# Kernel tuning notes

Measured on AMD Instinct MI355X. Metric: run time of the kernel, lower is better.

## Reference

```python
import jax, jax.numpy as jnp
import numpy as np

H0, W0 = 256, 256
B = 8
N_EV = 100000
N_PARAMS = 4000000
SMOOTHNESS_WEIGHT = 0.5
WEIGHT_DECAY_WEIGHT = 1e-4


def setup_inputs() -> dict:
    key = jax.random.key(0)
    ks = jax.random.split(key, 11)
    d = {}
    for i in range(4):
        s = 2 ** (3 - i)
        d['flow%d' % i] = jax.random.normal(ks[i], (B, 2, H0 // s, W0 // s), jnp.float32)
    d['xs'] = jax.random.randint(ks[4], (B, N_EV), 0, W0).astype(jnp.int32)
    d['ys'] = jax.random.randint(ks[5], (B, N_EV), 0, H0).astype(jnp.int32)
    # timestamps sorted ascending so t[-1]/t[0] are the last/first event times
    d['ts'] = jnp.sort(jax.random.uniform(ks[6], (B, N_EV), jnp.float32), axis=1)
    # polarity in {-1, +1}
    d['ps'] = (2 * jax.random.randint(ks[7], (B, N_EV), 0, 2) - 1).astype(jnp.int32)
    d['frame'] = jax.random.normal(ks[8], (B, 1, H0, W0), jnp.float32)
    d['frame_'] = jax.random.normal(ks[9], (B, 1, H0, W0), jnp.float32)
    d['params'] = jax.random.normal(ks[10], (N_PARAMS,), jnp.float32) * 0.01
    return d


def _event_loss(x, y, t, mask, flow, forward):
    # x, y: int32 [N] in-range coords for this flow scale; t: float [N];
    # mask: bool [N] selecting the polarity subset; flow: [2, H, W].
    # Masked events contribute zero weight instead of being sliced out
    # (shape-stable equivalent of torch boolean indexing).
    eps = jnp.finfo(flow.dtype).eps
    H, W = flow.shape[1], flow.shape[2]
    n = t.shape[0]
    mf = mask.astype(flow.dtype)
    if forward:
        t_ref = t[n - 1 - jnp.argmax(mask[::-1])]  # t[-1] of masked subset
        t_ = t_ref - t + eps
    else:
        t_ref = t[jnp.argmax(mask)]  # t[0] of masked subset
        t_ = t_ref - t - eps
    fx = flow[0, y, x]
    fy = flow[1, y, x]
    x_ = jnp.clip(x.astype(flow.dtype) + t_ * fx, 0.0, W - 1.0)
    y_ = jnp.clip(y.astype(flow.dtype) + t_ * fy, 0.0, H - 1.0)
    x0 = jnp.floor(x_); x1 = x0 + 1.0
    y0 = jnp.floor(y_); y1 = y0 + 1.0
    x0w = x_ - x0; x1w = x1 - x_
    y0w = y_ - y0; y1w = y1 - y_
    tm = t * mf
    Ta = x0w * y0w * tm
    Tb = x1w * y0w * tm
    Tc = x0w * y1w * tm
    Td = x1w * y1w * tm
    x1i = jnp.minimum(x1, W - 1.0).astype(jnp.int32)
    y1i = jnp.minimum(y1, H - 1.0).astype(jnp.int32)
    x0i = x0.astype(jnp.int32); y0i = y0.astype(jnp.int32)
    Ia = x1i + y1i * W
    Ib = x0i + y1i * W
    Ic = x1i + y0i * W
    Id = x0i + y0i * W
    idxs = jnp.concatenate([Ia, Ib, Ic, Id])
    vals = jnp.concatenate([Ta, Tb, Tc, Td])
    den = jnp.zeros(H * W, flow.dtype).at[idxs].add(jnp.tile(mf, 4))
    num = jnp.zeros(H * W, flow.dtype).at[idxs].add(vals)
    r = num / (den + eps)
    return jnp.sum(jnp.sqrt(r * r + 1e-06))


def _compute_event_flow_loss(xs, ys, ts, ps, flows):
    total = jnp.float32(0.0)
    pos = ps == 1
    neg = ps == -1
    for fi, flow in enumerate(flows):  # 4 scales, structurally distinct shapes
        scale = 2 ** (3 - fi)
        x = (xs.astype(jnp.float32) / scale).astype(jnp.int32)
        y = (ys.astype(jnp.float32) / scale).astype(jnp.int32)
        for mask in (pos, neg):
            for fwd in (True, False):
                f = lambda xb, yb, tb, mb, fb, fwd=fwd: _event_loss(xb, yb, tb, mb, fb, fwd)
                total = total + jnp.sum(jax.vmap(f)(x, y, ts, mask, flow))
    return total


def _charbonnier(d):
    # alpha=0.45, epsilon=1e-3 -> epsilon**2 = 1e-6
    return jnp.mean((d * d + 1e-06) ** 0.45)


def _smoothness(flow):
    lr = _charbonnier(flow[..., :, 1:] - flow[..., :, :-1])
    ud = _charbonnier(flow[..., 1:, :] - flow[..., :-1, :])
    d1 = _charbonnier(flow[..., 1:, 1:] - flow[..., :-1, :-1])
    d2 = _charbonnier(flow[..., :-1, 1:] - flow[..., 1:, :-1])
    return (lr + ud + d1 + d2) / 4.0


def reference(flow0, flow1, flow2, flow3, xs, ys, ts, ps, frame, frame_, params):
    flows = [flow0, flow1, flow2, flow3]
    weight_decay_loss = jnp.sum(params ** 2) / 2.0 * WEIGHT_DECAY_WEIGHT
    smoothness_loss = sum(_smoothness(f) for f in flows) * (SMOOTHNESS_WEIGHT / 4.0)
    event_loss = _compute_event_flow_loss(xs, ys, ts, ps, flows)
    return weight_decay_loss + event_loss + smoothness_loss * 200.0
```

## Files before the change

### kernel.cpp

```cpp
#include <hip/hip_runtime.h>
#include <math.h>
#include <limits.h>

#define NEV 100000
#define NB 8
#define NSL 32
#define SLEV (NEV / NSL)
#define F32EPS 1.1920929e-7f
#define SCALE 524288.0f
#define INV_SCALE (1.0f/524288.0f)

typedef unsigned long long u64;

#define BINS_BYTES 6400000
#define OFF_BINSTART 6400000
#define OFF_TREF     6401056
#define OFF_FI0P     6401184
#define OFF_FI1P     8498336
#define OFF_HISTG    12692640
#define OFF_CURSG    12823712
#define OFF_MMG      12954784

__device__ __forceinline__ void lds_add64(u64* p, u64 v) {
    __hip_atomic_fetch_add(p, v, __ATOMIC_RELAXED, __HIP_MEMORY_SCOPE_WORKGROUP);
}
__device__ __forceinline__ int lds_add32(int* p, int v) {
    return __hip_atomic_fetch_add(p, v, __ATOMIC_RELAXED, __HIP_MEMORY_SCOPE_WORKGROUP);
}

__global__ __launch_bounds__(256) void k_hist(
    const int* __restrict__ ys, const int* __restrict__ ps,
    int* __restrict__ histG, int* __restrict__ mmG) {
    int bid = blockIdx.x;
    int b = bid & 7;
    int sl = bid >> 3;
    int tid = threadIdx.x;
    int w = tid >> 6, lane = tid & 63;

    const int* yb = ys + b * NEV + sl * SLEV;
    const int* pb = ps + b * NEV + sl * SLEV;

    __shared__ int hist[4][32];
    __shared__ int mm[4];
    if (tid < 128) hist[tid >> 5][tid & 31] = 0;
    if (tid == 0) { mm[0] = INT_MAX; mm[1] = -1; mm[2] = INT_MAX; mm[3] = -1; }
    __syncthreads();

    int mnP = INT_MAX, mxP = -1, mnN = INT_MAX, mxN = -1;
    int gbase = sl * SLEV;
    for (int i = w * 64 + lane; i < SLEV; i += 256) {
        int p = pb[i];
        int y = yb[i];
        int m = (p == 1) ? 0 : 1;
        lds_add32(&hist[w][m * 16 + (y >> 4)], 1);
        int gi = gbase + i;
        if (m == 0) { mnP = min(mnP, gi); mxP = max(mxP, gi); }
        else        { mnN = min(mnN, gi); mxN = max(mxN, gi); }
    }
    for (int o = 32; o > 0; o >>= 1) {
        mnP = min(mnP, __shfl_down(mnP, o, 64));
        mxP = max(mxP, __shfl_down(mxP, o, 64));
        mnN = min(mnN, __shfl_down(mnN, o, 64));
        mxN = max(mxN, __shfl_down(mxN, o, 64));
    }
    if (lane == 0) {
        atomicMin(&mm[0], mnP); atomicMax(&mm[1], mxP);
        atomicMin(&mm[2], mnN); atomicMax(&mm[3], mxN);
    }
    __syncthreads();
    if (tid < 128) histG[(bid * 4 + (tid >> 5)) * 32 + (tid & 31)] = hist[tid >> 5][tid & 31];
    if (tid < 4)   mmG[bid * 4 + tid] = mm[tid];
}

__global__ __launch_bounds__(256) void k_scan(
    const int* __restrict__ histG, const int* __restrict__ mmG,
    const float* __restrict__ ts,
    int* __restrict__ cursG, int* __restrict__ binStart,
    float* __restrict__ tref, float* __restrict__ out) {
    int tid = threadIdx.x;
    int b = tid >> 5, bin = tid & 31;
    __shared__ int tot[8][32];
    __shared__ int bs[8][33];

    int s = 0;
    for (int sl = 0; sl < NSL; ++sl) {
        int bid = sl * 8 + b;
        #pragma unroll
        for (int w = 0; w < 4; ++w) s += histG[(bid * 4 + w) * 32 + bin];
    }
    tot[b][bin] = s;
    __syncthreads();

    if (tid < 8) {
        int run = 0;
        for (int k = 0; k < 32; ++k) { bs[tid][k] = run; run += tot[tid][k]; }
        bs[tid][32] = run;
    }
    __syncthreads();
    if (bin == 0 && b == 0) out[0] = 0.0f;
    binStart[b * 33 + bin] = bs[b][bin];
    if (tid < 8) binStart[tid * 33 + 32] = bs[tid][32];

    int run = bs[b][bin];
    for (int sl = 0; sl < NSL; ++sl) {
        int bid = sl * 8 + b;
        #pragma unroll
        for (int w = 0; w < 4; ++w) {
            int idx = (bid * 4 + w) * 32 + bin;
            int h = histG[idx];
            cursG[idx] = run;
            run += h;
        }
    }

    if (tid < 8) {
        int mnP = INT_MAX, mxP = -1, mnN = INT_MAX, mxN = -1;
        for (int sl = 0; sl < NSL; ++sl) {
            const int* m = mmG + (sl * 8 + tid) * 4;
            mnP = min(mnP, m[0]); mxP = max(mxP, m[1]);
            mnN = min(mnN, m[2]); mxN = max(mxN, m[3]);
        }
        const float* tb = ts + tid * NEV;
        int fP = (mnP == INT_MAX) ? 0 : mnP;
        int lP = (mxP < 0) ? (NEV - 1) : mxP;
        int fN = (mnN == INT_MAX) ? 0 : mnN;
        int lN = (mxN < 0) ? (NEV - 1) : mxN;
        tref[tid * 4 + 0] = tb[lP];
        tref[tid * 4 + 1] = tb[fP];
        tref[tid * 4 + 2] = tb[lN];
        tref[tid * 4 + 3] = tb[fN];
    }
}

__global__ __launch_bounds__(256) void k_scatter(
    const int* __restrict__ xs, const int* __restrict__ ys,
    const float* __restrict__ ts, const int* __restrict__ ps,
    const int* __restrict__ cursG, uint2* __restrict__ bins) {
    int bid = blockIdx.x;
    int b = bid & 7;
    int sl = bid >> 3;
    int tid = threadIdx.x;
    int w = tid >> 6, lane = tid & 63;

    const int*   xb = xs + b * NEV + sl * SLEV;
    const int*   yb = ys + b * NEV + sl * SLEV;
    const float* tb = ts + b * NEV + sl * SLEV;
    const int*   pb = ps + b * NEV + sl * SLEV;
    uint2* ob = bins + b * NEV;

    __shared__ int curs[4][32];
    if (tid < 128) curs[tid >> 5][tid & 31] = cursG[(bid * 4 + (tid >> 5)) * 32 + (tid & 31)];
    __syncthreads();

    for (int i = w * 64 + lane; i < SLEV; i += 256) {
        int p = pb[i];
        int x = xb[i];
        int y = yb[i];
        float t = tb[i];
        int m = (p == 1) ? 0 : 1;
        int bin = m * 16 + (y >> 4);
        int pos = lds_add32(&curs[w][bin], 1);
        ob[pos] = make_uint2((unsigned)(x | (y << 8)), __float_as_uint(t));
    }
}

__global__ __launch_bounds__(1024) void k_splat(
    const float* __restrict__ f0, const float* __restrict__ f1,
    const float* __restrict__ f2, const float* __restrict__ f3,
    const uint2* __restrict__ bins, const int* __restrict__ binStart,
    const float* __restrict__ tref,
    u64* __restrict__ fi0P, u64* __restrict__ fi1P,
    float* __restrict__ out) {
    __shared__ u64 acc[8192];
    __shared__ float red[16];

    int tid = threadIdx.x;
    int bid = blockIdx.x;
    int b = bid & 7;
    int rm = bid >> 3;
    int m = rm & 1;
    int role = rm >> 1;
    int bm = b * 2 + m;

    int fi, row0 = 0, nrows, lo, hi, slice = 0, nslice = 1, mode;
    if (role < 8)       { fi = 0; mode = 0; slice = role;      nslice = 8; nrows = 32; lo = 0; hi = 15; }
    else if (role < 12) { fi = 1; mode = 0; slice = role - 8;  nslice = 4; nrows = 64; lo = 0; hi = 15; }
    else if (role < 20) { int c = role - 12; fi = 2; mode = 1; row0 = 16 * c; nrows = 16;
                          lo = max(0, 2 * c - 1); hi = min(15, 2 * c + 2); }
    else                { int c = role - 20; fi = 3; mode = 1; row0 = 16 * c; nrows = 16;
                          lo = max(0, c - 1); hi = min(15, c + 1); }

    int W = 32 << fi;
    int sh = 3 - fi;
    int planeN = (fi == 0) ? 1024 : (fi == 1) ? 4096 : nrows * W;
    int used = (fi == 0) ? 8192 : 2 * planeN;
    int rowEnd = row0 + nrows;
    float Wm1 = (float)(W - 1);

    const float* flow = (fi == 0) ? f0 : (fi == 1) ? f1 : (fi == 2) ? f2 : f3;
    const float* fxp = flow + (size_t)b * 2 * W * W;
    const float* fyp = fxp + W * W;

    for (int i = tid; i < used; i += 1024) acc[i] = 0ULL;
    __syncthreads();

    float trF = tref[b * 4 + m * 2 + 0];
    float trB = tref[b * 4 + m * 2 + 1];

    int s0 = binStart[b * 33 + m * 16 + lo];
    int e0 = binStart[b * 33 + m * 16 + hi + 1];
    const uint2* eb = bins + b * NEV;

    int rep = (fi == 0) ? (((tid >> 4) & 3) * 2048) : 0;

    for (int i = s0 + slice * 1024 + tid; i < e0; i += nslice * 1024) {
        uint2 ev = eb[i];
        int x = ev.x & 255;
        int y = (ev.x >> 8) & 255;
        float t = __uint_as_float(ev.y);
        int xi = x >> sh, yi = y >> sh;
        float fx = fxp[yi * W + xi];
        float fy = fyp[yi * W + xi];
        float tF = trF - t + F32EPS;
        float tB = trB - t - F32EPS;
        #pragma unroll
        for (int dir = 0; dir < 2; ++dir) {
            float t_ = dir ? tB : tF;
            float x_ = fminf(fmaxf((float)xi + t_ * fx, 0.0f), Wm1);
            float y_ = fminf(fmaxf((float)yi + t_ * fy, 0.0f), Wm1);
            float x0f = floorf(x_), y0f = floorf(y_);
            float x0w = x_ - x0f, x1w = 1.0f - x0w;
            float y0w = y_ - y0f, y1w = 1.0f - y0w;
            int x0i = (int)x0f, y0i = (int)y0f;
            int x1i = min(x0i + 1, W - 1);
            int y1i = min(y0i + 1, W - 1);
            u64 Pa = (1ULL << 32) | (u64)(unsigned)(x0w * y0w * t * SCALE);
            u64 Pb = (1ULL << 32) | (u64)(unsigned)(x1w * y0w * t * SCALE);
            u64 Pc = (1ULL << 32) | (u64)(unsigned)(x0w * y1w * t * SCALE);
            u64 Pd = (1ULL << 32) | (u64)(unsigned)(x1w * y1w * t * SCALE);
            int base = rep + dir * planeN;
            if (mode == 0) {
                int r1 = base + y1i * W;
                int r0 = base + y0i * W;
                lds_add64(&acc[r1 + x1i], Pa);
                lds_add64(&acc[r1 + x0i], Pb);
                lds_add64(&acc[r0 + x1i], Pc);
                lds_add64(&acc[r0 + x0i], Pd);
            } else {
                if (y1i >= row0 && y1i < rowEnd) {
                    int r = base + (y1i - row0) * W;
                    lds_add64(&acc[r + x1i], Pa);
                    lds_add64(&acc[r + x0i], Pb);
                }
                if (y0i >= row0 && y0i < rowEnd) {
                    int r = base + (y0i - row0) * W;
                    lds_add64(&acc[r + x1i], Pc);
                    lds_add64(&acc[r + x0i], Pd);
                }
            }
        }
    }
    __syncthreads();

    if (mode == 0) {
        if (fi == 0) {
            for (int j = tid; j < 2048; j += 1024)
                fi0P[(bm * 8 + slice) * 2048 + j] =
                    acc[j] + acc[j + 2048] + acc[j + 4096] + acc[j + 6144];
        } else {
            for (int j = tid; j < 8192; j += 1024)
                fi1P[(bm * 4 + slice) * 8192 + j] = acc[j];
        }
        return;
    }

    float s = 0.0f;
    for (int j = tid; j < used; j += 1024) {
        u64 v = acc[j];
        float num = (float)(unsigned)(v & 0xffffffffULL) * INV_SCALE;
        float den = (float)(unsigned)(v >> 32);
        float r = num / (den + F32EPS);
        s += sqrtf(r * r + 1e-6f);
    }
    for (int o = 32; o > 0; o >>= 1) s += __shfl_down(s, o, 64);
    if ((tid & 63) == 0) red[tid >> 6] = s;
    __syncthreads();
    if (tid == 0) {
        float tot = 0.0f;
        for (int w2 = 0; w2 < 16; ++w2) tot += red[w2];
        atomicAdd(out, tot);
    }
}

__global__ __launch_bounds__(256) void k_merge(const u64* __restrict__ fi0P,
                                               const u64* __restrict__ fi1P,
                                               float* __restrict__ out) {
    int idx = blockIdx.x * 256 + threadIdx.x;
    u64 v = 0;
    if (idx < 32768) {
        int bm = idx >> 11, j = idx & 2047;
        const u64* p = fi0P + (bm * 8) * 2048 + j;
        #pragma unroll
        for (int s = 0; s < 8; ++s) v += p[s * 2048];
    } else {
        int r = idx - 32768;
        int bm = r >> 13, j = r & 8191;
        const u64* p = fi1P + (bm * 4) * 8192 + j;
        #pragma unroll
        for (int s = 0; s < 4; ++s) v += p[s * 8192];
    }
    float num = (float)(unsigned)(v & 0xffffffffULL) * INV_SCALE;
    float den = (float)(unsigned)(v >> 32);
    float r = num / (den + F32EPS);
    float s = sqrtf(r * r + 1e-6f);
    for (int o = 32; o > 0; o >>= 1) s += __shfl_down(s, o, 64);
    __shared__ float red[4];
    if ((threadIdx.x & 63) == 0) red[threadIdx.x >> 6] = s;
    __syncthreads();
    if (threadIdx.x == 0)
        atomicAdd(out, red[0] + red[1] + red[2] + red[3]);
}

__global__ __launch_bounds__(256) void k_misc(
    const float* __restrict__ params, int nP,
    const float* __restrict__ f0, const float* __restrict__ f1,
    const float* __restrict__ f2, const float* __restrict__ f3,
    float* __restrict__ out) {
    float s = 0.0f;
    int gstride = gridDim.x * blockDim.x;
    int gtid = blockIdx.x * blockDim.x + threadIdx.x;

    int n4 = nP >> 2;
    const float4* p4 = (const float4*)params;
    float w = 0.0f;
    for (int i = gtid; i < n4; i += gstride) {
        float4 v = p4[i];
        w += v.x * v.x + v.y * v.y + v.z * v.z + v.w * v.w;
    }
    if (gtid == 0) for (int i = n4 * 4; i < nP; ++i) w += params[i] * params[i];
    s += w * 5e-5f;

    const int nTot = 1392640;
    for (int idx = gtid; idx < nTot; idx += gstride) {
        int fi, off, logW;
        if (idx < 16384)       { fi = 0; off = 0;      logW = 5; }
        else if (idx < 81920)  { fi = 1; off = 16384;  logW = 6; }
        else if (idx < 344064) { fi = 2; off = 81920;  logW = 7; }
        else                   { fi = 3; off = 344064; logW = 8; }
        const float* f = (fi == 0) ? f0 : (fi == 1) ? f1 : (fi == 2) ? f2 : f3;
        int W = 1 << logW;
        int local = idx - off;
        int x = local & (W - 1);
        int y = (local >> logW) & (W - 1);
        float c_lr = 6.25f / (float)(16 * W * (W - 1));
        float c_dd = 6.25f / (float)(16 * (W - 1) * (W - 1));
        float v = f[local];
        bool xok = x < W - 1;
        bool yok = y < W - 1;
        float vr = xok ? f[local + 1] : 0.0f;
        float vd = yok ? f[local + W] : 0.0f;
        if (xok) { float d = vr - v; s += c_lr * __powf(d * d + 1e-6f, 0.45f); }
        if (yok) { float d = vd - v; s += c_lr * __powf(d * d + 1e-6f, 0.45f); }
        if (xok && yok) {
            float d1 = f[local + W + 1] - v;
            s += c_dd * __powf(d1 * d1 + 1e-6f, 0.45f);
            float d2 = vr - vd;
            s += c_dd * __powf(d2 * d2 + 1e-6f, 0.45f);
        }
    }

    for (int o = 32; o > 0; o >>= 1) s += __shfl_down(s, o, 64);
    __shared__ float red[4];
    if ((threadIdx.x & 63) == 0) red[threadIdx.x >> 6] = s;
    __syncthreads();
    if (threadIdx.x == 0)
        atomicAdd(out, red[0] + red[1] + red[2] + red[3]);
}

extern "C" void kernel_launch(void* const* d_in, const int* in_sizes, int n_in,
                              void* d_out, int out_size, void* d_ws, size_t ws_size,
                              hipStream_t stream) {
    const float* f0 = (const float*)d_in[0];
    const float* f1 = (const float*)d_in[1];
    const float* f2 = (const float*)d_in[2];
    const float* f3 = (const float*)d_in[3];
    const int*   xs = (const int*)d_in[4];
    const int*   ys = (const int*)d_in[5];
    const float* ts = (const float*)d_in[6];
    const int*   ps = (const int*)d_in[7];
    const float* params = (const float*)d_in[10];
    float* out = (float*)d_out;

    char* ws = (char*)d_ws;
    uint2* bins     = (uint2*)ws;
    int*   binStart = (int*)(ws + OFF_BINSTART);
    float* tref     = (float*)(ws + OFF_TREF);
    u64*   fi0P     = (u64*)(ws + OFF_FI0P);
    u64*   fi1P     = (u64*)(ws + OFF_FI1P);
    int*   histG    = (int*)(ws + OFF_HISTG);
    int*   cursG    = (int*)(ws + OFF_CURSG);
    int*   mmG      = (int*)(ws + OFF_MMG);

    hipLaunchKernelGGL(k_hist, dim3(NB * NSL), dim3(256), 0, stream, ys, ps, histG, mmG);
    hipLaunchKernelGGL(k_scan, dim3(1), dim3(256), 0, stream,
                       histG, mmG, ts, cursG, binStart, tref, out);
    hipLaunchKernelGGL(k_scatter, dim3(NB * NSL), dim3(256), 0, stream,
                       xs, ys, ts, ps, cursG, bins);
    hipLaunchKernelGGL(k_splat, dim3(576), dim3(1024), 0, stream,
                       f0, f1, f2, f3, bins, binStart, tref, fi0P, fi1P, out);
    hipLaunchKernelGGL(k_merge, dim3(640), dim3(256), 0, stream, fi0P, fi1P, out);
    hipLaunchKernelGGL(k_misc, dim3(1024), dim3(256), 0, stream,
                       params, in_sizes[10], f0, f1, f2, f3, out);
}
```

Before: 182.6 us.

## Fuse all six passes into one cooperative kernel with grid syncs

Replaces the six separate launches (hist, scan, scatter, splat, merge, misc) with a single cooperative kernel of 256 blocks of 1024 threads, separated by grid-wide syncs. The scan runs on 8 blocks while the other blocks compute weight decay and smoothness concurrently, and the splat work is repartitioned into two units per block with fewer slices for the coarsest scale. This removes kernel launch gaps and the serial single-block scan stall. In exchange it adds grid-sync costs, and every phase is limited to 256 co-resident blocks.

```diff
diff --git a/kernel.cpp b/kernel.cpp
--- a/kernel.cpp
+++ b/kernel.cpp
@@ -1,9 +1,11 @@
 #include <hip/hip_runtime.h>
+#include <hip/hip_cooperative_groups.h>
 #include <math.h>
 #include <limits.h>
 
+namespace cg = cooperative_groups;
+
 #define NEV 100000
-#define NB 8
 #define NSL 32
 #define SLEV (NEV / NSL)
 #define F32EPS 1.1920929e-7f
@@ -12,14 +14,13 @@
 
 typedef unsigned long long u64;
 
-#define BINS_BYTES 6400000
 #define OFF_BINSTART 6400000
 #define OFF_TREF     6401056
 #define OFF_FI0P     6401184
-#define OFF_FI1P     8498336
-#define OFF_HISTG    12692640
-#define OFF_CURSG    12823712
-#define OFF_MMG      12954784
+#define OFF_FI1P     7449760
+#define OFF_HISTG    11644064
+#define OFF_CURSG    12168352
+#define OFF_MMB      12692640
 
 __device__ __forceinline__ void lds_add64(u64* p, u64 v) {
     __hip_atomic_fetch_add(p, v, __ATOMIC_RELAXED, __HIP_MEMORY_SCOPE_WORKGROUP);
@@ -28,353 +29,345 @@
     return __hip_atomic_fetch_add(p, v, __ATOMIC_RELAXED, __HIP_MEMORY_SCOPE_WORKGROUP);
 }
 
-__global__ __launch_bounds__(256) void k_hist(
-    const int* __restrict__ ys, const int* __restrict__ ps,
-    int* __restrict__ histG, int* __restrict__ mmG) {
-    int bid = blockIdx.x;
-    int b = bid & 7;
-    int sl = bid >> 3;
-    int tid = threadIdx.x;
-    int w = tid >> 6, lane = tid & 63;
-
-    const int* yb = ys + b * NEV + sl * SLEV;
-    const int* pb = ps + b * NEV + sl * SLEV;
-
-    __shared__ int hist[4][32];
-    __shared__ int mm[4];
-    if (tid < 128) hist[tid >> 5][tid & 31] = 0;
-    if (tid == 0) { mm[0] = INT_MAX; mm[1] = -1; mm[2] = INT_MAX; mm[3] = -1; }
-    __syncthreads();
-
-    int mnP = INT_MAX, mxP = -1, mnN = INT_MAX, mxN = -1;
-    int gbase = sl * SLEV;
-    for (int i = w * 64 + lane; i < SLEV; i += 256) {
-        int p = pb[i];
-        int y = yb[i];
-        int m = (p == 1) ? 0 : 1;
-        lds_add32(&hist[w][m * 16 + (y >> 4)], 1);
-        int gi = gbase + i;
-        if (m == 0) { mnP = min(mnP, gi); mxP = max(mxP, gi); }
-        else        { mnN = min(mnN, gi); mxN = max(mxN, gi); }
-    }
-    for (int o = 32; o > 0; o >>= 1) {
-        mnP = min(mnP, __shfl_down(mnP, o, 64));
-        mxP = max(mxP, __shfl_down(mxP, o, 64));
-        mnN = min(mnN, __shfl_down(mnN, o, 64));
-        mxN = max(mxN, __shfl_down(mxN, o, 64));
-    }
-    if (lane == 0) {
-        atomicMin(&mm[0], mnP); atomicMax(&mm[1], mxP);
-        atomicMin(&mm[2], mnN); atomicMax(&mm[3], mxN);
-    }
-    __syncthreads();
-    if (tid < 128) histG[(bid * 4 + (tid >> 5)) * 32 + (tid & 31)] = hist[tid >> 5][tid & 31];
-    if (tid < 4)   mmG[bid * 4 + tid] = mm[tid];
-}
-
-__global__ __launch_bounds__(256) void k_scan(
-    const int* __restrict__ histG, const int* __restrict__ mmG,
-    const float* __restrict__ ts,
-    int* __restrict__ cursG, int* __restrict__ binStart,
-    float* __restrict__ tref, float* __restrict__ out) {
-    int tid = threadIdx.x;
-    int b = tid >> 5, bin = tid & 31;
-    __shared__ int tot[8][32];
-    __shared__ int bs[8][33];
-
-    int s = 0;
-    for (int sl = 0; sl < NSL; ++sl) {
-        int bid = sl * 8 + b;
-        #pragma unroll
-        for (int w = 0; w < 4; ++w) s += histG[(bid * 4 + w) * 32 + bin];
-    }
-    tot[b][bin] = s;
-    __syncthreads();
-
-    if (tid < 8) {
-        int run = 0;
-        for (int k = 0; k < 32; ++k) { bs[tid][k] = run; run += tot[tid][k]; }
-        bs[tid][32] = run;
-    }
-    __syncthreads();
-    if (bin == 0 && b == 0) out[0] = 0.0f;
-    binStart[b * 33 + bin] = bs[b][bin];
-    if (tid < 8) binStart[tid * 33 + 32] = bs[tid][32];
-
-    int run = bs[b][bin];
-    for (int sl = 0; sl < NSL; ++sl) {
-        int bid = sl * 8 + b;
-        #pragma unroll
-        for (int w = 0; w < 4; ++w) {
-            int idx = (bid * 4 + w) * 32 + bin;
-            int h = histG[idx];
-            cursG[idx] = run;
-            run += h;
-        }
-    }
-
-    if (tid < 8) {
-        int mnP = INT_MAX, mxP = -1, mnN = INT_MAX, mxN = -1;
-        for (int sl = 0; sl < NSL; ++sl) {
-            const int* m = mmG + (sl * 8 + tid) * 4;
-            mnP = min(mnP, m[0]); mxP = max(mxP, m[1]);
-            mnN = min(mnN, m[2]); mxN = max(mxN, m[3]);
-        }
-        const float* tb = ts + tid * NEV;
-        int fP = (mnP == INT_MAX) ? 0 : mnP;
-        int lP = (mxP < 0) ? (NEV - 1) : mxP;
-        int fN = (mnN == INT_MAX) ? 0 : mnN;
-        int lN = (mxN < 0) ? (NEV - 1) : mxN;
-        tref[tid * 4 + 0] = tb[lP];
-        tref[tid * 4 + 1] = tb[fP];
-        tref[tid * 4 + 2] = tb[lN];
-        tref[tid * 4 + 3] = tb[fN];
-    }
-}
-
-__global__ __launch_bounds__(256) void k_scatter(
+__global__ __launch_bounds__(1024, 4) void k_fused(
+    const float* __restrict__ f0, const float* __restrict__ f1,
+    const float* __restrict__ f2, const float* __restrict__ f3,
     const int* __restrict__ xs, const int* __restrict__ ys,
     const float* __restrict__ ts, const int* __restrict__ ps,
-    const int* __restrict__ cursG, uint2* __restrict__ bins) {
-    int bid = blockIdx.x;
-    int b = bid & 7;
-    int sl = bid >> 3;
-    int tid = threadIdx.x;
-    int w = tid >> 6, lane = tid & 63;
-
-    const int*   xb = xs + b * NEV + sl * SLEV;
-    const int*   yb = ys + b * NEV + sl * SLEV;
-    const float* tb = ts + b * NEV + sl * SLEV;
-    const int*   pb = ps + b * NEV + sl * SLEV;
-    uint2* ob = bins + b * NEV;
-
-    __shared__ int curs[4][32];
-    if (tid < 128) curs[tid >> 5][tid & 31] = cursG[(bid * 4 + (tid >> 5)) * 32 + (tid & 31)];
-    __syncthreads();
-
-    for (int i = w * 64 + lane; i < SLEV; i += 256) {
-        int p = pb[i];
-        int x = xb[i];
-        int y = yb[i];
-        float t = tb[i];
-        int m = (p == 1) ? 0 : 1;
-        int bin = m * 16 + (y >> 4);
-        int pos = lds_add32(&curs[w][bin], 1);
-        ob[pos] = make_uint2((unsigned)(x | (y << 8)), __float_as_uint(t));
+    const float* __restrict__ params, int nP,
+    uint2* __restrict__ bins, int* __restrict__ binStart,
+    float* __restrict__ tref, u64* __restrict__ fi0P, u64* __restrict__ fi1P,
+    int* __restrict__ histG, int* __restrict__ cursG, int* __restrict__ mmB,
+    float* __restrict__ out)
+{
+    cg::grid_group grid = cg::this_grid();
+    __shared__ u64 acc[8192];
+    int*   shi = (int*)acc;
+    float* shf = (float*)acc;
+
+    const int tid  = threadIdx.x;
+    const int bid  = blockIdx.x;
+    const int w    = tid >> 6;
+    const int lane = tid & 63;
+
+    {
+        const int b = bid & 7, sl = bid >> 3;
+        const int* yb = ys + b * NEV + sl * SLEV;
+        const int* pb = ps + b * NEV + sl * SLEV;
+        if (tid < 512) shi[tid] = 0;
+        if (tid >= 512 && tid < 516) shi[tid] = (tid & 1) ? -1 : INT_MAX;
+        if (bid == 0 && tid == 1023) out[0] = 0.0f;
+        __syncthreads();
+
+        int mnP = INT_MAX, mxP = -1, mnN = INT_MAX, mxN = -1;
+        const int gbase = sl * SLEV;
+        for (int i = tid; i < SLEV; i += 1024) {
+            int p = pb[i], y = yb[i];
+            int m = (p == 1) ? 0 : 1;
+            lds_add32(&shi[w * 32 + m * 16 + (y >> 4)], 1);
+            int gi = gbase + i;
+            if (m == 0) { mnP = min(mnP, gi); mxP = max(mxP, gi); }
+            else        { mnN = min(mnN, gi); mxN = max(mxN, gi); }
+        }
+        for (int o = 32; o > 0; o >>= 1) {
+            mnP = min(mnP, __shfl_down(mnP, o, 64));
+            mxP = max(mxP, __shfl_down(mxP, o, 64));
+            mnN = min(mnN, __shfl_down(mnN, o, 64));
+            mxN = max(mxN, __shfl_down(mxN, o, 64));
+        }
+        if (lane == 0) {
+            atomicMin(&shi[512], mnP); atomicMax(&shi[513], mxP);
+            atomicMin(&shi[514], mnN); atomicMax(&shi[515], mxN);
+        }
+        __syncthreads();
+        if (tid < 512) histG[bid * 512 + tid] = shi[tid];
+        if (tid < 4)   mmB[bid * 4 + tid] = shi[512 + tid];
     }
-}
-
-__global__ __launch_bounds__(1024) void k_splat(
-    const float* __restrict__ f0, const float* __restrict__ f1,
-    const float* __restrict__ f2, const float* __restrict__ f3,
-    const uint2* __restrict__ bins, const int* __restrict__ binStart,
-    const float* __restrict__ tref,
-    u64* __restrict__ fi0P, u64* __restrict__ fi1P,
-    float* __restrict__ out) {
-    __shared__ u64 acc[8192];
-    __shared__ float red[16];
-
-    int tid = threadIdx.x;
-    int bid = blockIdx.x;
-    int b = bid & 7;
-    int rm = bid >> 3;
-    int m = rm & 1;
-    int role = rm >> 1;
-    int bm = b * 2 + m;
-
-    int fi, row0 = 0, nrows, lo, hi, slice = 0, nslice = 1, mode;
-    if (role < 8)       { fi = 0; mode = 0; slice = role;      nslice = 8; nrows = 32; lo = 0; hi = 15; }
-    else if (role < 12) { fi = 1; mode = 0; slice = role - 8;  nslice = 4; nrows = 64; lo = 0; hi = 15; }
-    else if (role < 20) { int c = role - 12; fi = 2; mode = 1; row0 = 16 * c; nrows = 16;
-                          lo = max(0, 2 * c - 1); hi = min(15, 2 * c + 2); }
-    else                { int c = role - 20; fi = 3; mode = 1; row0 = 16 * c; nrows = 16;
-                          lo = max(0, c - 1); hi = min(15, c + 1); }
-
-    int W = 32 << fi;
-    int sh = 3 - fi;
-    int planeN = (fi == 0) ? 1024 : (fi == 1) ? 4096 : nrows * W;
-    int used = (fi == 0) ? 8192 : 2 * planeN;
-    int rowEnd = row0 + nrows;
-    float Wm1 = (float)(W - 1);
-
-    const float* flow = (fi == 0) ? f0 : (fi == 1) ? f1 : (fi == 2) ? f2 : f3;
-    const float* fxp = flow + (size_t)b * 2 * W * W;
-    const float* fyp = fxp + W * W;
-
-    for (int i = tid; i < used; i += 1024) acc[i] = 0ULL;
-    __syncthreads();
-
-    float trF = tref[b * 4 + m * 2 + 0];
-    float trB = tref[b * 4 + m * 2 + 1];
-
-    int s0 = binStart[b * 33 + m * 16 + lo];
-    int e0 = binStart[b * 33 + m * 16 + hi + 1];
-    const uint2* eb = bins + b * NEV;
-
-    int rep = (fi == 0) ? (((tid >> 4) & 3) * 2048) : 0;
-
-    for (int i = s0 + slice * 1024 + tid; i < e0; i += nslice * 1024) {
-        uint2 ev = eb[i];
-        int x = ev.x & 255;
-        int y = (ev.x >> 8) & 255;
-        float t = __uint_as_float(ev.y);
-        int xi = x >> sh, yi = y >> sh;
-        float fx = fxp[yi * W + xi];
-        float fy = fyp[yi * W + xi];
-        float tF = trF - t + F32EPS;
-        float tB = trB - t - F32EPS;
+    grid.sync();
+
+    if (bid < 8) {
+        const int b = bid;
+        const int sl = tid >> 5, bin = tid & 31;
+        int s = 0;
         #pragma unroll
-        for (int dir = 0; dir < 2; ++dir) {
-            float t_ = dir ? tB : tF;
-            float x_ = fminf(fmaxf((float)xi + t_ * fx, 0.0f), Wm1);
-            float y_ = fminf(fmaxf((float)yi + t_ * fy, 0.0f), Wm1);
-            float x0f = floorf(x_), y0f = floorf(y_);
-            float x0w = x_ - x0f, x1w = 1.0f - x0w;
-            float y0w = y_ - y0f, y1w = 1.0f - y0w;
-            int x0i = (int)x0f, y0i = (int)y0f;
-            int x1i = min(x0i + 1, W - 1);
-            int y1i = min(y0i + 1, W - 1);
-            u64 Pa = (1ULL << 32) | (u64)(unsigned)(x0w * y0w * t * SCALE);
-            u64 Pb = (1ULL << 32) | (u64)(unsigned)(x1w * y0w * t * SCALE);
-            u64 Pc = (1ULL << 32) | (u64)(unsigned)(x0w * y1w * t * SCALE);
-            u64 Pd = (1ULL << 32) | (u64)(unsigned)(x1w * y1w * t * SCALE);
-            int base = rep + dir * planeN;
-            if (mode == 0) {
-                int r1 = base + y1i * W;
-                int r0 = base + y0i * W;
-                lds_add64(&acc[r1 + x1i], Pa);
-                lds_add64(&acc[r1 + x0i], Pb);
-                lds_add64(&acc[r0 + x1i], Pc);
-                lds_add64(&acc[r0 + x0i], Pd);
+        for (int wv = 0; wv < 16; ++wv)
+            s += histG[((sl * 8 + b) * 16 + wv) * 32 + bin];
+        shi[sl * 32 + bin] = s;
+        __syncthreads();
+        if (tid < 32) {
+            int run = 0;
+            for (int g = 0; g < 32; ++g) {
+                int v = shi[g * 32 + tid];
+                shi[1024 + g * 32 + tid] = run; run += v;
+            }
+            shi[2048 + tid] = run;
+        }
+        __syncthreads();
+        if (tid == 0) {
+            int run = 0;
+            for (int k = 0; k < 32; ++k) {
+                shi[2080 + k] = run; binStart[b * 33 + k] = run;
+                run += shi[2048 + k];
+            }
+            binStart[b * 33 + 32] = run;
+        }
+        __syncthreads();
+        {
+            int run = shi[2080 + bin] + shi[1024 + sl * 32 + bin];
+            #pragma unroll
+            for (int wv = 0; wv < 16; ++wv) {
+                int idx = ((sl * 8 + b) * 16 + wv) * 32 + bin;
+                int h = histG[idx];
+                cursG[idx] = run; run += h;
+            }
+        }
+        if (tid < 4) {
+            int c = tid;
+            int v = (c == 0 || c == 2) ? INT_MAX : -1;
+            for (int sl2 = 0; sl2 < 32; ++sl2) {
+                int x = mmB[(sl2 * 8 + b) * 4 + c];
+                v = (c == 0 || c == 2) ? min(v, x) : max(v, x);
+            }
+            shi[2112 + c] = v;
+        }
+        __syncthreads();
+        if (tid == 0) {
+            const float* tb = ts + b * NEV;
+            int mnP = shi[2112], mxP = shi[2113], mnN = shi[2114], mxN = shi[2115];
+            int fP = (mnP == INT_MAX) ? 0 : mnP;
+            int lP = (mxP < 0) ? (NEV - 1) : mxP;
+            int fN = (mnN == INT_MAX) ? 0 : mnN;
+            int lN = (mxN < 0) ? (NEV - 1) : mxN;
+            tref[b * 4 + 0] = tb[lP];
+            tref[b * 4 + 1] = tb[fP];
+            tref[b * 4 + 2] = tb[lN];
+            tref[b * 4 + 3] = tb[fN];
+        }
+    } else {
+        float s = 0.0f;
+        const int gtid = (bid - 8) * 1024 + tid;
+        const int gstride = 248 * 1024;
+
+        int n4 = nP >> 2;
+        const float4* p4 = (const float4*)params;
+        float wsum = 0.0f;
+        for (int i = gtid; i < n4; i += gstride) {
+            float4 v = p4[i];
+            wsum += v.x * v.x + v.y * v.y + v.z * v.z + v.w * v.w;
+        }
+        if (gtid == 0) for (int i = n4 * 4; i < nP; ++i) wsum += params[i] * params[i];
+        s += wsum * 5e-5f;
+
+        const int nTot = 1392640;
+        for (int idx = gtid; idx < nTot; idx += gstride) {
+            int fi, off, logW;
+            if (idx < 16384)       { fi = 0; off = 0;      logW = 5; }
+            else if (idx < 81920)  { fi = 1; off = 16384;  logW = 6; }
+            else if (idx < 344064) { fi = 2; off = 81920;  logW = 7; }
+            else                   { fi = 3; off = 344064; logW = 8; }
+            const float* f = (fi == 0) ? f0 : (fi == 1) ? f1 : (fi == 2) ? f2 : f3;
+            int W = 1 << logW;
+            int local = idx - off;
+            int x = local & (W - 1);
+            int y = (local >> logW) & (W - 1);
+            float c_lr = 6.25f / (float)(16 * W * (W - 1));
+            float c_dd = 6.25f / (float)(16 * (W - 1) * (W - 1));
+            float v = f[local];
+            bool xok = x < W - 1;
+            bool yok = y < W - 1;
+            float vr = xok ? f[local + 1] : 0.0f;
+            float vd = yok ? f[local + W] : 0.0f;
+            if (xok) { float d = vr - v; s += c_lr * __powf(d * d + 1e-6f, 0.45f); }
+            if (yok) { float d = vd - v; s += c_lr * __powf(d * d + 1e-6f, 0.45f); }
+            if (xok && yok) {
+                float d1 = f[local + W + 1] - v;
+                s += c_dd * __powf(d1 * d1 + 1e-6f, 0.45f);
+                float d2 = vr - vd;
+                s += c_dd * __powf(d2 * d2 + 1e-6f, 0.45f);
+            }
+        }
+        for (int o = 32; o > 0; o >>= 1) s += __shfl_down(s, o, 64);
+        __syncthreads();
+        if (lane == 0) shf[w] = s;
+        __syncthreads();
+        if (tid == 0) {
+            float tot = 0.0f;
+            for (int k = 0; k < 16; ++k) tot += shf[k];
+            atomicAdd(out, tot);
+        }
+    }
+    grid.sync();
+
+    {
+        const int b = bid & 7, sl = bid >> 3;
+        const int*   xb  = xs + b * NEV + sl * SLEV;
+        const int*   yb  = ys + b * NEV + sl * SLEV;
+        const float* tb2 = ts + b * NEV + sl * SLEV;
+        const int*   pb  = ps + b * NEV + sl * SLEV;
+        uint2* ob = bins + b * NEV;
+
+        if (tid < 512) shi[tid] = cursG[bid * 512 + tid];
+        __syncthreads();
+        for (int i = tid; i < SLEV; i += 1024) {
+            int p = pb[i], x = xb[i], y = yb[i];
+            float t = tb2[i];
+            int m = (p == 1) ? 0 : 1;
+            int bin = m * 16 + (y >> 4);
+            int pos = lds_add32(&shi[w * 32 + bin], 1);
+            ob[pos] = make_uint2((unsigned)(x | (y << 8)), __float_as_uint(t));
+        }
+    }
+    grid.sync();
+
+    for (int u = 0; u < 2; ++u) {
+        const int unit = bid + u * 256;
+        const int b = unit & 7;
+        const int rm = unit >> 3;
+        const int m = rm & 1;
+        const int role = rm >> 1;
+        const int bm = b * 2 + m;
+
+        int fi, row0 = 0, nrows, lo, hi, slice = 0, nslice = 1, mode;
+        if (role < 4)       { fi = 0; mode = 0; slice = role;     nslice = 4; nrows = 32; lo = 0; hi = 15; }
+        else if (role < 8)  { fi = 1; mode = 0; slice = role - 4; nslice = 4; nrows = 64; lo = 0; hi = 15; }
+        else if (role < 16) { int c = role - 8;  fi = 2; mode = 1; row0 = 16 * c; nrows = 16;
+                              lo = max(0, 2 * c - 1); hi = min(15, 2 * c + 2); }
+        else                { int c = role - 16; fi = 3; mode = 1; row0 = 16 * c; nrows = 16;
+                              lo = max(0, c - 1); hi = min(15, c + 1); }
+
+        const int W = 32 << fi;
+        const int sh = 3 - fi;
+        const int planeN = (fi == 0) ? 1024 : (fi == 1) ? 4096 : nrows * W;
+        const int used = (fi == 0) ? 8192 : 2 * planeN;
+        const int rowEnd = row0 + nrows;
+        const float Wm1 = (float)(W - 1);
+
+        const float* flow = (fi == 0) ? f0 : (fi == 1) ? f1 : (fi == 2) ? f2 : f3;
+        const float* fxp = flow + (size_t)b * 2 * W * W;
+        const float* fyp = fxp + W * W;
+
+        __syncthreads();
+        for (int i = tid; i < used; i += 1024) acc[i] = 0ULL;
+        __syncthreads();
+
+        const float trF = tref[b * 4 + m * 2 + 0];
+        const float trB = tref[b * 4 + m * 2 + 1];
+        const int s0 = binStart[b * 33 + m * 16 + lo];
+        const int e0 = binStart[b * 33 + m * 16 + hi + 1];
+        const uint2* eb = bins + b * NEV;
+        const int rep = (fi == 0) ? (((tid >> 4) & 3) * 2048) : 0;
+
+        for (int i = s0 + slice * 1024 + tid; i < e0; i += nslice * 1024) {
+            uint2 ev = eb[i];
+            int x = ev.x & 255;
+            int y = (ev.x >> 8) & 255;
+            float t = __uint_as_float(ev.y);
+            int xi = x >> sh, yi = y >> sh;
+            float fx = fxp[yi * W + xi];
+            float fy = fyp[yi * W + xi];
+            float tF = trF - t + F32EPS;
+            float tB = trB - t - F32EPS;
+            #pragma unroll
+            for (int dir = 0; dir < 2; ++dir) {
+                float t_ = dir ? tB : tF;
+                float x_ = fminf(fmaxf((float)xi + t_ * fx, 0.0f), Wm1);
+                float y_ = fminf(fmaxf((float)yi + t_ * fy, 0.0f), Wm1);
+                float x0f = floorf(x_), y0f = floorf(y_);
+                float x0w = x_ - x0f, x1w = 1.0f - x0w;
+                float y0w = y_ - y0f, y1w = 1.0f - y0w;
+                int x0i = (int)x0f, y0i = (int)y0f;
+                int x1i = min(x0i + 1, W - 1);
+                int y1i = min(y0i + 1, W - 1);
+                u64 Pa = (1ULL << 32) | (u64)(unsigned)(x0w * y0w * t * SCALE);
+                u64 Pb = (1ULL << 32) | (u64)(unsigned)(x1w * y0w * t * SCALE);
+                u64 Pc = (1ULL << 32) | (u64)(unsigned)(x0w * y1w * t * SCALE);
+                u64 Pd = (1ULL << 32) | (u64)(unsigned)(x1w * y1w * t * SCALE);
+                int base = rep + dir * planeN;
+                if (mode == 0) {
+                    int r1 = base + y1i * W;
+                    int r0 = base + y0i * W;
+                    lds_add64(&acc[r1 + x1i], Pa);
+                    lds_add64(&acc[r1 + x0i], Pb);
+                    lds_add64(&acc[r0 + x1i], Pc);
+                    lds_add64(&acc[r0 + x0i], Pd);
+                } else {
+                    if (y1i >= row0 && y1i < rowEnd) {
+                        int r = base + (y1i - row0) * W;
+                        lds_add64(&acc[r + x1i], Pa);
+                        lds_add64(&acc[r + x0i], Pb);
+                    }
+                    if (y0i >= row0 && y0i < rowEnd) {
+                        int r = base + (y0i - row0) * W;
+                        lds_add64(&acc[r + x1i], Pc);
+                        lds_add64(&acc[r + x0i], Pd);
+                    }
+                }
+            }
+        }
+        __syncthreads();
+
+        if (mode == 0) {
+            if (fi == 0) {
+                for (int j = tid; j < 2048; j += 1024)
+                    fi0P[(bm * 4 + slice) * 2048 + j] =
+                        acc[j] + acc[j + 2048] + acc[j + 4096] + acc[j + 6144];
             } else {
-                if (y1i >= row0 && y1i < rowEnd) {
-                    int r = base + (y1i - row0) * W;
-                    lds_add64(&acc[r + x1i], Pa);
-                    lds_add64(&acc[r + x0i], Pb);
-                }
-                if (y0i >= row0 && y0i < rowEnd) {
-                    int r = base + (y0i - row0) * W;
-                    lds_add64(&acc[r + x1i], Pc);
-                    lds_add64(&acc[r + x0i], Pd);
-                }
+                for (int j = tid; j < 8192; j += 1024)
+                    fi1P[(bm * 4 + slice) * 8192 + j] = acc[j];
+            }
+        } else {
+            float s = 0.0f;
+            for (int j = tid; j < used; j += 1024) {
+                u64 v = acc[j];
+                float num = (float)(unsigned)(v & 0xffffffffULL) * INV_SCALE;
+                float den = (float)(unsigned)(v >> 32);
+                float r = num / (den + F32EPS);
+                s += sqrtf(r * r + 1e-6f);
+            }
+            for (int o = 32; o > 0; o >>= 1) s += __shfl_down(s, o, 64);
+            __syncthreads();
+            if (lane == 0) shf[w] = s;
+            __syncthreads();
+            if (tid == 0) {
+                float tot = 0.0f;
+                for (int k = 0; k < 16; ++k) tot += shf[k];
+                atomicAdd(out, tot);
             }
         }
     }
-    __syncthreads();
-
-    if (mode == 0) {
-        if (fi == 0) {
-            for (int j = tid; j < 2048; j += 1024)
-                fi0P[(bm * 8 + slice) * 2048 + j] =
-                    acc[j] + acc[j + 2048] + acc[j + 4096] + acc[j + 6144];
-        } else {
-            for (int j = tid; j < 8192; j += 1024)
-                fi1P[(bm * 4 + slice) * 8192 + j] = acc[j];
-        }
-        return;
+    grid.sync();
+
+    {
+        const int idx = bid * 1024 + tid;
+        if (idx < 163840) {
+            u64 v = 0;
+            if (idx < 32768) {
+                int bm = idx >> 11, j = idx & 2047;
+                const u64* p = fi0P + (bm * 4) * 2048 + j;
+                #pragma unroll
+                for (int s2 = 0; s2 < 4; ++s2) v += p[s2 * 2048];
+            } else {
+                int r = idx - 32768;
+                int bm = r >> 13, j = r & 8191;
+                const u64* p = fi1P + (bm * 4) * 8192 + j;
+                #pragma unroll
+                for (int s2 = 0; s2 < 4; ++s2) v += p[s2 * 8192];
+            }
+            float num = (float)(unsigned)(v & 0xffffffffULL) * INV_SCALE;
+            float den = (float)(unsigned)(v >> 32);
+            float r2 = num / (den + F32EPS);
+            float sv = sqrtf(r2 * r2 + 1e-6f);
+            for (int o = 32; o > 0; o >>= 1) sv += __shfl_down(sv, o, 64);
+            __syncthreads();
+            if (lane == 0) shf[w] = sv;
+            __syncthreads();
+            if (tid == 0) {
+                float tot = 0.0f;
+                for (int k = 0; k < 16; ++k) tot += shf[k];
+                atomicAdd(out, tot);
+            }
+        }
     }
-
-    float s = 0.0f;
-    for (int j = tid; j < used; j += 1024) {
-        u64 v = acc[j];
-        float num = (float)(unsigned)(v & 0xffffffffULL) * INV_SCALE;
-        float den = (float)(unsigned)(v >> 32);
-        float r = num / (den + F32EPS);
-        s += sqrtf(r * r + 1e-6f);
-    }
-    for (int o = 32; o > 0; o >>= 1) s += __shfl_down(s, o, 64);
-    if ((tid & 63) == 0) red[tid >> 6] = s;
-    __syncthreads();
-    if (tid == 0) {
-        float tot = 0.0f;
-        for (int w2 = 0; w2 < 16; ++w2) tot += red[w2];
-        atomicAdd(out, tot);
-    }
-}
-
-__global__ __launch_bounds__(256) void k_merge(const u64* __restrict__ fi0P,
-                                               const u64* __restrict__ fi1P,
-                                               float* __restrict__ out) {
-    int idx = blockIdx.x * 256 + threadIdx.x;
-    u64 v = 0;
-    if (idx < 32768) {
-        int bm = idx >> 11, j = idx & 2047;
-        const u64* p = fi0P + (bm * 8) * 2048 + j;
-        #pragma unroll
-        for (int s = 0; s < 8; ++s) v += p[s * 2048];
-    } else {
-        int r = idx - 32768;
-        int bm = r >> 13, j = r & 8191;
-        const u64* p = fi1P + (bm * 4) * 8192 + j;
-        #pragma unroll
-        for (int s = 0; s < 4; ++s) v += p[s * 8192];
-    }
-    float num = (float)(unsigned)(v & 0xffffffffULL) * INV_SCALE;
-    float den = (float)(unsigned)(v >> 32);
-    float r = num / (den + F32EPS);
-    float s = sqrtf(r * r + 1e-6f);
-    for (int o = 32; o > 0; o >>= 1) s += __shfl_down(s, o, 64);
-    __shared__ float red[4];
-    if ((threadIdx.x & 63) == 0) red[threadIdx.x >> 6] = s;
-    __syncthreads();
-    if (threadIdx.x == 0)
-        atomicAdd(out, red[0] + red[1] + red[2] + red[3]);
-}
-
-__global__ __launch_bounds__(256) void k_misc(
-    const float* __restrict__ params, int nP,
-    const float* __restrict__ f0, const float* __restrict__ f1,
-    const float* __restrict__ f2, const float* __restrict__ f3,
-    float* __restrict__ out) {
-    float s = 0.0f;
-    int gstride = gridDim.x * blockDim.x;
-    int gtid = blockIdx.x * blockDim.x + threadIdx.x;
-
-    int n4 = nP >> 2;
-    const float4* p4 = (const float4*)params;
-    float w = 0.0f;
-    for (int i = gtid; i < n4; i += gstride) {
-        float4 v = p4[i];
-        w += v.x * v.x + v.y * v.y + v.z * v.z + v.w * v.w;
-    }
-    if (gtid == 0) for (int i = n4 * 4; i < nP; ++i) w += params[i] * params[i];
-    s += w * 5e-5f;
-
-    const int nTot = 1392640;
-    for (int idx = gtid; idx < nTot; idx += gstride) {
-        int fi, off, logW;
-        if (idx < 16384)       { fi = 0; off = 0;      logW = 5; }
-        else if (idx < 81920)  { fi = 1; off = 16384;  logW = 6; }
-        else if (idx < 344064) { fi = 2; off = 81920;  logW = 7; }
-        else                   { fi = 3; off = 344064; logW = 8; }
-        const float* f = (fi == 0) ? f0 : (fi == 1) ? f1 : (fi == 2) ? f2 : f3;
-        int W = 1 << logW;
-        int local = idx - off;
-        int x = local & (W - 1);
-        int y = (local >> logW) & (W - 1);
-        float c_lr = 6.25f / (float)(16 * W * (W - 1));
-        float c_dd = 6.25f / (float)(16 * (W - 1) * (W - 1));
-        float v = f[local];
-        bool xok = x < W - 1;
-        bool yok = y < W - 1;
-        float vr = xok ? f[local + 1] : 0.0f;
-        float vd = yok ? f[local + W] : 0.0f;
-        if (xok) { float d = vr - v; s += c_lr * __powf(d * d + 1e-6f, 0.45f); }
-        if (yok) { float d = vd - v; s += c_lr * __powf(d * d + 1e-6f, 0.45f); }
-        if (xok && yok) {
-            float d1 = f[local + W + 1] - v;
-            s += c_dd * __powf(d1 * d1 + 1e-6f, 0.45f);
-            float d2 = vr - vd;
-            s += c_dd * __powf(d2 * d2 + 1e-6f, 0.45f);
-        }
-    }
-
-    for (int o = 32; o > 0; o >>= 1) s += __shfl_down(s, o, 64);
-    __shared__ float red[4];
-    if ((threadIdx.x & 63) == 0) red[threadIdx.x >> 6] = s;
-    __syncthreads();
-    if (threadIdx.x == 0)
-        atomicAdd(out, red[0] + red[1] + red[2] + red[3]);
 }
 
 extern "C" void kernel_launch(void* const* d_in, const int* in_sizes, int n_in,
@@ -389,6 +382,7 @@
     const float* ts = (const float*)d_in[6];
     const int*   ps = (const int*)d_in[7];
     const float* params = (const float*)d_in[10];
+    int nP = in_sizes[10];
     float* out = (float*)d_out;
 
     char* ws = (char*)d_ws;
@@ -399,16 +393,13 @@
     u64*   fi1P     = (u64*)(ws + OFF_FI1P);
     int*   histG    = (int*)(ws + OFF_HISTG);
     int*   cursG    = (int*)(ws + OFF_CURSG);
-    int*   mmG      = (int*)(ws + OFF_MMG);
-
-    hipLaunchKernelGGL(k_hist, dim3(NB * NSL), dim3(256), 0, stream, ys, ps, histG, mmG);
-    hipLaunchKernelGGL(k_scan, dim3(1), dim3(256), 0, stream,
-                       histG, mmG, ts, cursG, binStart, tref, out);
-    hipLaunchKernelGGL(k_scatter, dim3(NB * NSL), dim3(256), 0, stream,
-                       xs, ys, ts, ps, cursG, bins);
-    hipLaunchKernelGGL(k_splat, dim3(576), dim3(1024), 0, stream,
-                       f0, f1, f2, f3, bins, binStart, tref, fi0P, fi1P, out);
-    hipLaunchKernelGGL(k_merge, dim3(640), dim3(256), 0, stream, fi0P, fi1P, out);
-    hipLaunchKernelGGL(k_misc, dim3(1024), dim3(256), 0, stream,
-                       params, in_sizes[10], f0, f1, f2, f3, out);
+    int*   mmB      = (int*)(ws + OFF_MMB);
+
+    void* args[] = { (void*)&f0, (void*)&f1, (void*)&f2, (void*)&f3,
+                     (void*)&xs, (void*)&ys, (void*)&ts, (void*)&ps,
+                     (void*)&params, (void*)&nP,
+                     (void*)&bins, (void*)&binStart, (void*)&tref,
+                     (void*)&fi0P, (void*)&fi1P, (void*)&histG, (void*)&cursG,
+                     (void*)&mmB, (void*)&out };
+    hipLaunchCooperativeKernel(k_fused, dim3(256), dim3(1024), args, 0, stream);
 }
```

New measurement: 292.2 us. 60.1% more time.

## Parallelize histogram scan per batch and rebalance splat work split

Applied to the files above, without the earlier changes.

The scan kernel moves from a single 256-thread block, which looped serially over all slices, to one 1024-thread block per batch. Each thread now handles one slice and bin, and two small serial prefix passes run in shared memory. The splat kernel drops from 8 to 4 slices for the finest flow scale, cutting grid size and partial-buffer traffic in the merge kernel. The cost is fewer blocks of parallel atomic splatting for scale 0, so each block handles more events and could become a longer tail.

```diff
diff --git a/kernel.cpp b/kernel.cpp
--- a/kernel.cpp
+++ b/kernel.cpp
@@ -12,14 +12,13 @@
 
 typedef unsigned long long u64;
 
-#define BINS_BYTES 6400000
 #define OFF_BINSTART 6400000
 #define OFF_TREF     6401056
 #define OFF_FI0P     6401184
-#define OFF_FI1P     8498336
-#define OFF_HISTG    12692640
-#define OFF_CURSG    12823712
-#define OFF_MMG      12954784
+#define OFF_FI1P     7449760
+#define OFF_HISTG    11644064
+#define OFF_CURSG    11775136
+#define OFF_MMG      11906208
 
 __device__ __forceinline__ void lds_add64(u64* p, u64 v) {
     __hip_atomic_fetch_add(p, v, __ATOMIC_RELAXED, __HIP_MEMORY_SCOPE_WORKGROUP);
@@ -72,63 +71,79 @@
     if (tid < 4)   mmG[bid * 4 + tid] = mm[tid];
 }
 
-__global__ __launch_bounds__(256) void k_scan(
+__global__ __launch_bounds__(1024) void k_scan(
     const int* __restrict__ histG, const int* __restrict__ mmG,
     const float* __restrict__ ts,
     int* __restrict__ cursG, int* __restrict__ binStart,
     float* __restrict__ tref, float* __restrict__ out) {
+    int b = blockIdx.x;
     int tid = threadIdx.x;
-    int b = tid >> 5, bin = tid & 31;
-    __shared__ int tot[8][32];
-    __shared__ int bs[8][33];
+    int sl = tid >> 5, bin = tid & 31;
+
+    __shared__ int seg[32][32];
+    __shared__ int segbase[32][32];
+    __shared__ int binTot[32];
+    __shared__ int binBase[33];
+    __shared__ int mm[4];
 
     int s = 0;
-    for (int sl = 0; sl < NSL; ++sl) {
-        int bid = sl * 8 + b;
-        #pragma unroll
-        for (int w = 0; w < 4; ++w) s += histG[(bid * 4 + w) * 32 + bin];
-    }
-    tot[b][bin] = s;
-    __syncthreads();
-
-    if (tid < 8) {
+    #pragma unroll
+    for (int w = 0; w < 4; ++w)
+        s += histG[((sl * 8 + b) * 4 + w) * 32 + bin];
+    seg[sl][bin] = s;
+    __syncthreads();
+
+    if (tid < 32) {
         int run = 0;
-        for (int k = 0; k < 32; ++k) { bs[tid][k] = run; run += tot[tid][k]; }
-        bs[tid][32] = run;
-    }
-    __syncthreads();
-    if (bin == 0 && b == 0) out[0] = 0.0f;
-    binStart[b * 33 + bin] = bs[b][bin];
-    if (tid < 8) binStart[tid * 33 + 32] = bs[tid][32];
-
-    int run = bs[b][bin];
-    for (int sl = 0; sl < NSL; ++sl) {
-        int bid = sl * 8 + b;
+        for (int g = 0; g < 32; ++g) {
+            segbase[g][tid] = run; run += seg[g][tid];
+        }
+        binTot[tid] = run;
+    }
+    __syncthreads();
+    if (tid == 0) {
+        int run = 0;
+        for (int k = 0; k < 32; ++k) {
+            binBase[k] = run; binStart[b * 33 + k] = run;
+            run += binTot[k];
+        }
+        binBase[32] = run;
+        binStart[b * 33 + 32] = run;
+    }
+    if (b == 0 && tid == 512) out[0] = 0.0f;
+    __syncthreads();
+
+    {
+        int run = binBase[bin] + segbase[sl][bin];
         #pragma unroll
         for (int w = 0; w < 4; ++w) {
-            int idx = (bid * 4 + w) * 32 + bin;
+            int idx = ((sl * 8 + b) * 4 + w) * 32 + bin;
             int h = histG[idx];
-            cursG[idx] = run;
-            run += h;
-        }
-    }
-
-    if (tid < 8) {
-        int mnP = INT_MAX, mxP = -1, mnN = INT_MAX, mxN = -1;
-        for (int sl = 0; sl < NSL; ++sl) {
-            const int* m = mmG + (sl * 8 + tid) * 4;
-            mnP = min(mnP, m[0]); mxP = max(mxP, m[1]);
-            mnN = min(mnN, m[2]); mxN = max(mxN, m[3]);
-        }
-        const float* tb = ts + tid * NEV;
+            cursG[idx] = run; run += h;
+        }
+    }
+
+    if (tid < 4) {
+        int c = tid;
+        int v = (c == 0 || c == 2) ? INT_MAX : -1;
+        for (int sl2 = 0; sl2 < 32; ++sl2) {
+            int x = mmG[(sl2 * 8 + b) * 4 + c];
+            v = (c == 0 || c == 2) ? min(v, x) : max(v, x);
+        }
+        mm[c] = v;
+    }
+    __syncthreads();
+    if (tid == 0) {
+        const float* tb = ts + b * NEV;
+        int mnP = mm[0], mxP = mm[1], mnN = mm[2], mxN = mm[3];
         int fP = (mnP == INT_MAX) ? 0 : mnP;
         int lP = (mxP < 0) ? (NEV - 1) : mxP;
         int fN = (mnN == INT_MAX) ? 0 : mnN;
         int lN = (mxN < 0) ? (NEV - 1) : mxN;
-        tref[tid * 4 + 0] = tb[lP];
-        tref[tid * 4 + 1] = tb[fP];
-        tref[tid * 4 + 2] = tb[lN];
-        tref[tid * 4 + 3] = tb[fN];
+        tref[b * 4 + 0] = tb[lP];
+        tref[b * 4 + 1] = tb[fP];
+        tref[b * 4 + 2] = tb[lN];
+        tref[b * 4 + 3] = tb[fN];
     }
 }
 
@@ -183,11 +198,11 @@
     int bm = b * 2 + m;
 
     int fi, row0 = 0, nrows, lo, hi, slice = 0, nslice = 1, mode;
-    if (role < 8)       { fi = 0; mode = 0; slice = role;      nslice = 8; nrows = 32; lo = 0; hi = 15; }
-    else if (role < 12) { fi = 1; mode = 0; slice = role - 8;  nslice = 4; nrows = 64; lo = 0; hi = 15; }
-    else if (role < 20) { int c = role - 12; fi = 2; mode = 1; row0 = 16 * c; nrows = 16;
+    if (role < 4)       { fi = 0; mode = 0; slice = role;     nslice = 4; nrows = 32; lo = 0; hi = 15; }
+    else if (role < 8)  { fi = 1; mode = 0; slice = role - 4; nslice = 4; nrows = 64; lo = 0; hi = 15; }
+    else if (role < 16) { int c = role - 8;  fi = 2; mode = 1; row0 = 16 * c; nrows = 16;
                           lo = max(0, 2 * c - 1); hi = min(15, 2 * c + 2); }
-    else                { int c = role - 20; fi = 3; mode = 1; row0 = 16 * c; nrows = 16;
+    else                { int c = role - 16; fi = 3; mode = 1; row0 = 16 * c; nrows = 16;
                           lo = max(0, c - 1); hi = min(15, c + 1); }
 
     int W = 32 << fi;
@@ -265,7 +280,7 @@
     if (mode == 0) {
         if (fi == 0) {
             for (int j = tid; j < 2048; j += 1024)
-                fi0P[(bm * 8 + slice) * 2048 + j] =
+                fi0P[(bm * 4 + slice) * 2048 + j] =
                     acc[j] + acc[j + 2048] + acc[j + 4096] + acc[j + 6144];
         } else {
             for (int j = tid; j < 8192; j += 1024)
@@ -299,9 +314,9 @@
     u64 v = 0;
     if (idx < 32768) {
         int bm = idx >> 11, j = idx & 2047;
-        const u64* p = fi0P + (bm * 8) * 2048 + j;
+        const u64* p = fi0P + (bm * 4) * 2048 + j;
         #pragma unroll
-        for (int s = 0; s < 8; ++s) v += p[s * 2048];
+        for (int s = 0; s < 4; ++s) v += p[s * 2048];
     } else {
         int r = idx - 32768;
         int bm = r >> 13, j = r & 8191;
@@ -402,11 +417,11 @@
     int*   mmG      = (int*)(ws + OFF_MMG);
 
     hipLaunchKernelGGL(k_hist, dim3(NB * NSL), dim3(256), 0, stream, ys, ps, histG, mmG);
-    hipLaunchKernelGGL(k_scan, dim3(1), dim3(256), 0, stream,
+    hipLaunchKernelGGL(k_scan, dim3(NB), dim3(1024), 0, stream,
                        histG, mmG, ts, cursG, binStart, tref, out);
     hipLaunchKernelGGL(k_scatter, dim3(NB * NSL), dim3(256), 0, stream,
                        xs, ys, ts, ps, cursG, bins);
-    hipLaunchKernelGGL(k_splat, dim3(576), dim3(1024), 0, stream,
+    hipLaunchKernelGGL(k_splat, dim3(512), dim3(1024), 0, stream,
                        f0, f1, f2, f3, bins, binStart, tref, fi0P, fi1P, out);
     hipLaunchKernelGGL(k_merge, dim3(640), dim3(256), 0, stream, fi0P, fi1P, out);
     hipLaunchKernelGGL(k_misc, dim3(1024), dim3(256), 0, stream,
```

After: 188.0 us. 2.9% more time.
